# Kernel optimization log

Measured on AMD Instinct MI355X. Metric: run time of the kernel, lower is better.

Reference implementation:

```python
import jax, jax.numpy as jnp
import numpy as np

N_QUBITS = 10
DIM = 2 ** N_QUBITS          # quantum state dimension
N_LAYERS = 8                 # QAOA circuit depth
B, D_IN, D_HID = 8192, 1024, 2048


def _build_hamiltonians(key):
    """Faithful to _create_cost_hamiltonian / _create_mixer_hamiltonian."""
    k1, k2 = jax.random.split(key)
    # cost: random diagonal * 0.1 plus 100 nearest-neighbour real couplings * 0.05
    diag = (jax.random.normal(k1, (DIM,)) * 0.1).astype(jnp.complex64)
    Hc = jnp.zeros((DIM, DIM), jnp.complex64).at[jnp.arange(DIM), jnp.arange(DIM)].set(diag)
    i = jnp.arange(100)
    j = (i + 1) % DIM
    c = (jax.random.normal(k2, (100,)) * 0.05).astype(jnp.complex64)
    Hc = Hc.at[i, j].set(c).at[j, i].set(jnp.conj(c))
    # mixer: sum of Pauli-X on every qubit -> H[i, i^(1<<q)] += 1
    idx = jnp.arange(DIM)
    Hm = jnp.zeros((DIM, DIM), jnp.complex64)
    for q in range(N_QUBITS):
        Hm = Hm.at[idx, idx ^ (1 << q)].add(1.0)
    return Hc, Hm


def setup_inputs() -> dict:
    key = jax.random.key(0)
    ks = jax.random.split(key, 8)
    Hc, Hm = _build_hamiltonians(ks[0])
    s = lambda k, *sh: jax.random.normal(k, sh, jnp.float32)
    return {
        "x": s(ks[1], B, D_IN),
        "W1": s(ks[2], D_IN, D_HID) * 0.02, "b1": jnp.zeros((D_HID,), jnp.float32),
        "W2": s(ks[3], D_HID, D_HID // 2) * 0.02, "b2": jnp.zeros((D_HID // 2,), jnp.float32),
        "Wq": s(ks[4], N_QUBITS, D_HID // 2) * 0.02, "bq": jnp.zeros((D_HID // 2,), jnp.float32),
        "Wo": s(ks[5], D_HID // 2, D_IN) * 0.02, "bo": jnp.zeros((D_IN,), jnp.float32),
        "circuit_params": s(ks[6], 2 * N_LAYERS),
        "Hc": Hc, "Hm": Hm,
    }


def _qaoa_params(circuit_params, Hc, Hm):
    """QuantumApproximateOptimizer.optimize_parameters: layered unitary evolution
    then a projective measurement mapped to +/-1 parameters."""
    state = jnp.full((DIM,), 1.0 / np.sqrt(DIM), jnp.complex64)
    for l in range(N_LAYERS):  # small fixed layer count -> Python loop OK
        gamma = circuit_params[2 * l].astype(jnp.complex64)
        beta = circuit_params[2 * l + 1].astype(jnp.complex64)
        state = jax.scipy.linalg.expm(-1j * gamma * Hc) @ state
        state = jax.scipy.linalg.expm(-1j * beta * Hm) @ state
    probs = jnp.abs(state) ** 2
    m = jax.random.categorical(jax.random.key(42), jnp.log(probs + 1e-30))
    # format(m, '0{n}b') is MSB-first
    bits = (m >> jnp.arange(N_QUBITS - 1, -1, -1)) & 1
    return bits.astype(jnp.float32) * 2.0 - 1.0  # +/-1 per qubit


def reference(x, W1, b1, W2, b2, Wq, bq, Wo, bo, circuit_params, Hc, Hm):
    # classical encoder: Linear -> ReLU -> Linear
    feat = jax.nn.relu(x @ W1 + b1) @ W2 + b2          # [B, D_HID//2]
    # quantum branch (batch independent)
    qp = _qaoa_params(circuit_params, Hc, Hm)          # [N_QUBITS]
    # surface-code error correction: correction_lookup only maps syndromes
    # '0000'/'1111' to qubit indices 23/24, which fail the `qubit_idx < param_dim`
    # guard for param_dim = N_QUBITS -> provably a no-op; qp unchanged.
    qf = qp @ Wq + bq                                  # [D_HID//2]
    return (feat + qf) @ Wo + bo                       # [B, D_IN]
```

## Files before the change

### kernel.cpp

```cpp
#include <hip/hip_runtime.h>
#include <hip/hip_bf16.h>
#include <stdint.h>

#define DIM 1024
#define NQ 10
#define NLAYERS 8
#define KTAYLOR 24
#define B_ROWS 8192
#define D_IN 1024
#define D_HID 2048
#define D_HALF 1024

typedef __bf16 bf16x8 __attribute__((ext_vector_type(8)));
typedef float f32x4 __attribute__((ext_vector_type(4)));

__device__ __forceinline__ float ldany(const void* p, size_t i, bool f32) {
  if (f32) return ((const float*)p)[i];
  return (float)((const __bf16*)p)[i];
}

__device__ __forceinline__ uint16_t f2bf_bits(float f) {
  __bf16 v = (__bf16)f;
  return *(uint16_t*)&v;
}

__global__ void detect_kernel(const uint32_t* __restrict__ w1raw,
                              const uint32_t* __restrict__ hc,
                              int* __restrict__ flags) {
  if (threadIdx.x == 0) {
    int cnt = 0;
    for (int i = 0; i < 256; ++i) {
      uint16_t h = (uint16_t)(w1raw[i] & 0xFFFFu);
      if (((h >> 7) & 0xFF) >= 0x80) cnt++;
    }
    flags[0] = (cnt > 32) ? 1 : 0;

    uint32_t w1 = hc[1] & 0x7FFFFFFFu;
    uint32_t w2 = hc[2] & 0x7FFFFFFFu;
    uint32_t w1025 = hc[1025] & 0x7FFFFFFFu;
    int code;
    if (w2 != 0u) code = 1;
    else if (w1 != 0u && (w1 >> 16) == 0u) code = 3;
    else if (w1025 != 0u) code = 2;
    else if (w1 != 0u) code = 4;
    else code = 0;
    flags[1] = code;
  }
}

__global__ __launch_bounds__(256) void convert_bf16(
    const void* __restrict__ src, size_t soff, __bf16* __restrict__ dst,
    int n, const int* __restrict__ flags) {
  int i = (blockIdx.x * 256 + threadIdx.x) * 8;
  if (i >= n) return;
  if (flags[0]) {
    const float* s = (const float*)src + soff + i;
#pragma unroll
    for (int j = 0; j < 8; ++j) dst[i + j] = (__bf16)s[j];
  } else {
    *(uint4*)(dst + i) = *(const uint4*)((const uint16_t*)src + soff + i);
  }
}

__device__ __forceinline__ uint32_t rotl32(uint32_t v, int d) {
  return (v << d) | (v >> (32 - d));
}

__device__ inline void threefry2x32(uint32_t k0, uint32_t k1, uint32_t& x0, uint32_t& x1) {
  uint32_t ks2 = k0 ^ k1 ^ 0x1BD11BDAu;
  x0 += k0; x1 += k1;
#define RND(r) { x0 += x1; x1 = rotl32(x1, r); x1 ^= x0; }
  RND(13) RND(15) RND(26) RND(6)
  x0 += k1; x1 += ks2 + 1u;
  RND(17) RND(29) RND(16) RND(24)
  x0 += ks2; x1 += k0 + 2u;
  RND(13) RND(15) RND(26) RND(6)
  x0 += k0; x1 += k1 + 3u;
  RND(17) RND(29) RND(16) RND(24)
  x0 += k1; x1 += ks2 + 4u;
  RND(13) RND(15) RND(26) RND(6)
  x0 += ks2; x1 += k0 + 5u;
#undef RND
}

__device__ __forceinline__ float gumbel_from_bits(uint32_t b) {
  float f = __uint_as_float((b >> 9) | 0x3f800000u) - 1.0f;
  float u = fmaxf(f, 1.17549435e-38f);
  return -logf(-logf(u));
}

struct cplx { double r, i; };
__device__ __forceinline__ cplx load_hc(const void* H, int code, size_t idx) {
  switch (code) {
    case 2: return {(double)((const float*)H)[idx], 0.0};
    case 3: {
      const uint16_t* h = (const uint16_t*)H;
      return {(double)__uint_as_float((uint32_t)h[2 * idx] << 16),
              (double)__uint_as_float((uint32_t)h[2 * idx + 1] << 16)};
    }
    case 4: {
      const double* d = (const double*)H;
      return {d[2 * idx], d[2 * idx + 1]};
    }
    default: {
      float2 v = ((const float2*)H)[idx];
      return {(double)v.x, (double)v.y};
    }
  }
}

__global__ __launch_bounds__(1024) void qaoa_kernel(
    const void* __restrict__ Hc_raw, const void* __restrict__ cp,
    const void* __restrict__ b1, const void* __restrict__ b2,
    const void* __restrict__ bq, const void* __restrict__ bo,
    const void* __restrict__ Wq, const int* __restrict__ flags,
    float* __restrict__ b1f, float* __restrict__ bias2, float* __restrict__ bof,
    int* __restrict__ diag) {
  __shared__ double2 Sb[2][DIM];
  __shared__ float red_v[16];
  __shared__ int   red_i[16];
  __shared__ float red_p[16];
  __shared__ int bm_sh;

  const int t = threadIdx.x;
  const int lane = t & 63, wave = t >> 6;
  const bool f32 = (flags[0] != 0);
  const int code = flags[1];

  cplx dg = load_hc(Hc_raw, code, (size_t)t * DIM + t);

  cplx tdg0{0,0}, tdg1{0,0}, tcu0{0,0}, tcu1{0,0}, tcd0{0,0}, tcd1{0,0};
  if (wave == 0 && lane <= 50) {
    const size_t e0 = 2 * lane, e1 = 2 * lane + 1;
    tdg0 = load_hc(Hc_raw, code, e0 * DIM + e0);
    tdg1 = load_hc(Hc_raw, code, e1 * DIM + e1);
    if (e0 <= 100) tcu0 = load_hc(Hc_raw, code, e0 * DIM + e0 + 1);
    if (e1 <= 100) tcu1 = load_hc(Hc_raw, code, e1 * DIM + e1 + 1);
    if (e0 >= 1 && e0 <= 100) tcd0 = load_hc(Hc_raw, code, e0 * DIM + e0 - 1);
    if (e1 <= 100) tcd1 = load_hc(Hc_raw, code, e1 * DIM + e1 - 1);
  }

  double ar = 0.03125, ai = 0.0;

  for (int l = 0; l < NLAYERS; ++l) {
    const double gamma = (double)ldany(cp, 2 * l, f32);
    const double beta  = (double)ldany(cp, 2 * l + 1, f32);

    Sb[0][t] = make_double2(ar, ai);
    __syncthreads();
    if (t >= 102) {
      double sn, cs;
      sincos(gamma * dg.r, &sn, &cs);
      double sc_ = exp(gamma * dg.i);
      double nr = sc_ * (ar * cs + ai * sn);
      double ni = sc_ * (ai * cs - ar * sn);
      ar = nr; ai = ni;
    } else if (wave == 0) {
      double p0r = 0, p0i = 0, p1r = 0, p1i = 0;
      if (lane <= 50) {
        double2 v0 = Sb[0][2 * lane], v1 = Sb[0][2 * lane + 1];
        p0r = v0.x; p0i = v0.y; p1r = v1.x; p1i = v1.y;
      }
      double y0r = p0r, y0i = p0i, y1r = p1r, y1i = p1i;
#pragma unroll 4
      for (int k = 1; k <= KTAYLOR; ++k) {
        double dnr = __shfl_up(p1r, 1), dni = __shfl_up(p1i, 1);
        double upr = __shfl_down(p0r, 1), upi = __shfl_down(p0i, 1);
        double h0r = tdg0.r * p0r - tdg0.i * p0i + tcu0.r * p1r - tcu0.i * p1i
                   + tcd0.r * dnr - tcd0.i * dni;
        double h0i = tdg0.r * p0i + tdg0.i * p0r + tcu0.r * p1i + tcu0.i * p1r
                   + tcd0.r * dni + tcd0.i * dnr;
        double h1r = tdg1.r * p1r - tdg1.i * p1i + tcu1.r * upr - tcu1.i * upi
                   + tcd1.r * p0r - tcd1.i * p0i;
        double h1i = tdg1.r * p1i + tdg1.i * p1r + tcu1.r * upi + tcu1.i * upr
                   + tcd1.r * p0i + tcd1.i * p0r;
        double s = gamma / (double)k;
        p0r = s * h0i; p0i = -s * h0r;
        p1r = s * h1i; p1i = -s * h1r;
        y0r += p0r; y0i += p0i; y1r += p1r; y1i += p1i;
      }
      if (lane <= 50) {
        Sb[0][2 * lane]     = make_double2(y0r, y0i);
        Sb[0][2 * lane + 1] = make_double2(y1r, y1i);
      }
    }
    __syncthreads();
    if (t <= 101) { double2 v = Sb[0][t]; ar = v.x; ai = v.y; }

    const double cb = cos(beta), sb_ = sin(beta);
#pragma unroll
    for (int q = 0; q < 6; ++q) {
      double br_ = __shfl_xor(ar, 1 << q);
      double bi_ = __shfl_xor(ai, 1 << q);
      double nr = cb * ar + sb_ * bi_;
      double ni = cb * ai - sb_ * br_;
      ar = nr; ai = ni;
    }
    int s = 0;
#pragma unroll
    for (int q = 6; q < 10; ++q) {
      Sb[s][t] = make_double2(ar, ai);
      __syncthreads();
      double2 b = Sb[s][t ^ (1 << q)];
      double nr = cb * ar + sb_ * b.y;
      double ni = cb * ai - sb_ * b.x;
      ar = nr; ai = ni;
      s ^= 1;
    }
  }

  double prob = ar * ar + ai * ai;
  float pv = (float)prob;
  float score;
  {
    float logit = (float)log(prob + 1e-30);
    uint32_t x0 = 0u, x1 = (uint32_t)t;
    threefry2x32(0u, 42u, x0, x1);
    score = logit + gumbel_from_bits(x0 ^ x1);
  }
  int idx = t;
#pragma unroll
  for (int off = 32; off >= 1; off >>= 1) {
    float ov = __shfl_down(score, off);
    int oi = __shfl_down(idx, off);
    pv += __shfl_down(pv, off);
    if (ov > score) { score = ov; idx = oi; }
  }
  if (lane == 0) { red_v[wave] = score; red_i[wave] = idx; red_p[wave] = pv; }
  __syncthreads();
  if (t == 0) {
    float best = red_v[0]; int bm = red_i[0]; float total = red_p[0];
    for (int w = 1; w < 16; ++w) {
      total += red_p[w];
      if (red_v[w] > best) { best = red_v[w]; bm = red_i[w]; }
    }
    bm_sh = bm;
    diag[0] = (!(total > 0.99f && total < 1.01f)) ? 1 : 0;
    diag[1] = bm;
  }
  __syncthreads();
  const int m = bm_sh;

  float acc = ldany(b2, t, f32) + ldany(bq, t, f32);
#pragma unroll
  for (int k = 0; k < NQ; ++k) {
    float qp = ((m >> (9 - k)) & 1) ? 1.f : -1.f;
    acc += qp * ldany(Wq, k * D_HALF + t, f32);
  }
  bias2[t] = acc;
  bof[t] = ldany(bo, t, f32);
  b1f[t] = ldany(b1, t, f32);
  b1f[t + 1024] = ldany(b1, t + 1024, f32);
}

__global__ void sentinel_kernel(const int* __restrict__ flags,
                                const int* __restrict__ diag,
                                float* __restrict__ out) {
  if (threadIdx.x == 0 && (diag[0] || flags[1] == 0)) {
    out[0] = 1048576.0f + 4194304.0f * (float)diag[0]
           + 65536.0f * (float)flags[1] + 16.0f * (float)diag[1];
  }
}

__global__ __launch_bounds__(256) void transpose_any(
    const void* __restrict__ in, uint16_t* __restrict__ out, int R, int C,
    const int* __restrict__ flags) {
  __shared__ uint16_t tile[32][33];
  const bool f32 = (flags[0] != 0);
  int bc = blockIdx.x * 32, br = blockIdx.y * 32;
  int x = threadIdx.x, y = threadIdx.y;
#pragma unroll
  for (int i = 0; i < 4; ++i) {
    int r = y * 4 + i;
    size_t idx = (size_t)(br + r) * C + bc + x;
    tile[r][x] = f32 ? f2bf_bits(((const float*)in)[idx])
                     : ((const uint16_t*)in)[idx];
  }
  __syncthreads();
#pragma unroll
  for (int i = 0; i < 4; ++i) {
    int c = y * 4 + i;
    out[(size_t)(bc + c) * R + br + x] = tile[x][c];
  }
}

template <bool RELU, bool OUTF32>
__global__ __launch_bounds__(256) void gemm_bt(
    const __bf16* __restrict__ A, const __bf16* __restrict__ Bt,
    const float* __restrict__ bias, void* __restrict__ Cout,
    int N, int K) {
  __shared__ __bf16 Als[128 * 32];
  __shared__ __bf16 Bls[128 * 32];

  const int tid = threadIdx.x;
  const int wave = tid >> 6, lane = tid & 63;
  const int m0 = blockIdx.y * 128, n0 = blockIdx.x * 128;
  const int wm = (wave >> 1) * 64, wn = (wave & 1) * 64;
  const int lm = lane & 15, quad = lane >> 4;

  f32x4 acc[4][4] = {};

  for (int k0 = 0; k0 < K; k0 += 32) {
#pragma unroll
    for (int r = 0; r < 2; ++r) {
      int e = r * 2048 + wave * 512 + lane * 8;
      int row = e >> 5, col = e & 31;
      const __bf16* gp = A + (size_t)(m0 + row) * K + k0 + col;
      __builtin_amdgcn_global_load_lds(
          (const __attribute__((address_space(1))) void*)gp,
          (__attribute__((address_space(3))) void*)(Als + r * 2048 + wave * 512),
          16, 0, 0);
    }
#pragma unroll
    for (int r = 0; r < 2; ++r) {
      int e = r * 2048 + wave * 512 + lane * 8;
      int row = e >> 5, col = e & 31;
      const __bf16* gp = Bt + (size_t)(n0 + row) * K + k0 + col;
      __builtin_amdgcn_global_load_lds(
          (const __attribute__((address_space(1))) void*)gp,
          (__attribute__((address_space(3))) void*)(Bls + r * 2048 + wave * 512),
          16, 0, 0);
    }
    __syncthreads();

    bf16x8 af[4], bfr[4];
#pragma unroll
    for (int i = 0; i < 4; ++i)
      af[i] = *(const bf16x8*)(Als + (wm + i * 16 + lm) * 32 + quad * 8);
#pragma unroll
    for (int i = 0; i < 4; ++i)
      bfr[i] = *(const bf16x8*)(Bls + (wn + i * 16 + lm) * 32 + quad * 8);

#pragma unroll
    for (int mi = 0; mi < 4; ++mi)
#pragma unroll
      for (int ni = 0; ni < 4; ++ni)
        acc[mi][ni] = __builtin_amdgcn_mfma_f32_16x16x32_bf16(
            af[mi], bfr[ni], acc[mi][ni], 0, 0, 0);
    __syncthreads();
  }

#pragma unroll
  for (int mi = 0; mi < 4; ++mi) {
#pragma unroll
    for (int ni = 0; ni < 4; ++ni) {
      int col = n0 + wn + ni * 16 + lm;
      float bv = bias[col];
#pragma unroll
      for (int r = 0; r < 4; ++r) {
        int row = m0 + wm + mi * 16 + quad * 4 + r;
        float v = acc[mi][ni][r] + bv;
        if (RELU) v = fmaxf(v, 0.f);
        size_t oi = (size_t)row * N + col;
        if (OUTF32) ((float*)Cout)[oi] = v;
        else        ((__bf16*)Cout)[oi] = (__bf16)v;
      }
    }
  }
}

extern "C" void kernel_launch(void* const* d_in, const int* in_sizes, int n_in,
                              void* d_out, int out_size, void* d_ws, size_t ws_size,
                              hipStream_t stream) {
  const void* x  = d_in[0];
  const void* W1 = d_in[1];
  const void* b1 = d_in[2];
  const void* W2 = d_in[3];
  const void* b2 = d_in[4];
  const void* Wq = d_in[5];
  const void* bq = d_in[6];
  const void* Wo = d_in[7];
  const void* bo = d_in[8];
  const void* cp = d_in[9];
  const void* Hc = d_in[10];
  float* out = (float*)d_out;

  char* ws = (char*)d_ws;
  float* b1f   = (float*)ws;
  float* bias2 = (float*)(ws + 8192);
  float* bof   = (float*)(ws + 12288);
  int*   flags = (int*)(ws + 16384);
  int*   diag  = (int*)(ws + 16384 + 64);
  __bf16* W1T = (__bf16*)(ws + 20480);
  __bf16* W2T = W1T + (size_t)2048 * 1024;
  __bf16* WoT = W2T + (size_t)2048 * 1024;
  const size_t head = 20480 + 10485760;
  int R = B_ROWS;
  while (R > 128 && head + (size_t)R * 8192 > ws_size) R >>= 1;
  __bf16* xc   = (__bf16*)(ws + head);
  __bf16* Hbuf = xc + (size_t)R * 1024;
  __bf16* Fbuf = Hbuf + (size_t)R * 2048;

  detect_kernel<<<1, 64, 0, stream>>>((const uint32_t*)W1, (const uint32_t*)Hc, flags);

  qaoa_kernel<<<1, 1024, 0, stream>>>(Hc, cp, b1, b2, bq, bo, Wq, flags,
                                      b1f, bias2, bof, diag);

  transpose_any<<<dim3(2048 / 32, 1024 / 32), dim3(32, 8), 0, stream>>>(
      W1, (uint16_t*)W1T, 1024, 2048, flags);
  transpose_any<<<dim3(1024 / 32, 2048 / 32), dim3(32, 8), 0, stream>>>(
      W2, (uint16_t*)W2T, 2048, 1024, flags);
  transpose_any<<<dim3(1024 / 32, 1024 / 32), dim3(32, 8), 0, stream>>>(
      Wo, (uint16_t*)WoT, 1024, 1024, flags);

  for (int off = 0; off < B_ROWS; off += R) {
    int nconv = R * 1024;
    convert_bf16<<<(nconv / 8 + 255) / 256, 256, 0, stream>>>(
        x, (size_t)off * D_IN, xc, nconv, flags);
    gemm_bt<true, false><<<dim3(D_HID / 128, R / 128), 256, 0, stream>>>(
        xc, W1T, b1f, Hbuf, D_HID, D_IN);
    gemm_bt<false, false><<<dim3(D_HALF / 128, R / 128), 256, 0, stream>>>(
        Hbuf, W2T, bias2, Fbuf, D_HALF, D_HID);
    gemm_bt<false, true><<<dim3(D_IN / 128, R / 128), 256, 0, stream>>>(
        Fbuf, WoT, bof, out + (size_t)off * D_IN, D_IN, D_HALF);
  }

  sentinel_kernel<<<1, 64, 0, stream>>>(flags, diag, out);
}
```

Before: 326.3 us.

## Double-buffer LDS tiles in GEMM and remap blocks across XCDs

Uses two LDS buffers per operand so the next K tile is fetched with global_load_lds while MFMAs consume the current one, hiding load latency. Also remaps the flat workgroup index so consecutive tiles land on the same XCD, which should improve L2 reuse. This doubles LDS use per block and may lower occupancy, and the remap assumes the block count is divisible by 8.

```diff
diff --git a/kernel.cpp b/kernel.cpp
--- a/kernel.cpp
+++ b/kernel.cpp
@@ -284,52 +284,63 @@
   }
 }
 
+__device__ __forceinline__ void stage_tile(
+    const __bf16* __restrict__ G, int row0, int K, int k0,
+    __bf16* lds, int wave, int lane) {
+#pragma unroll
+  for (int r = 0; r < 2; ++r) {
+    int e = r * 2048 + wave * 512 + lane * 8;
+    int row = e >> 5, col = e & 31;
+    const __bf16* gp = G + (size_t)(row0 + row) * K + k0 + col;
+    __builtin_amdgcn_global_load_lds(
+        (const __attribute__((address_space(1))) void*)gp,
+        (__attribute__((address_space(3))) void*)(lds + r * 2048 + wave * 512),
+        16, 0, 0);
+  }
+}
+
 template <bool RELU, bool OUTF32>
 __global__ __launch_bounds__(256) void gemm_bt(
     const __bf16* __restrict__ A, const __bf16* __restrict__ Bt,
     const float* __restrict__ bias, void* __restrict__ Cout,
     int N, int K) {
-  __shared__ __bf16 Als[128 * 32];
-  __shared__ __bf16 Bls[128 * 32];
+  __shared__ __bf16 Als[2][128 * 32];
+  __shared__ __bf16 Bls[2][128 * 32];
 
   const int tid = threadIdx.x;
   const int wave = tid >> 6, lane = tid & 63;
-  const int m0 = blockIdx.y * 128, n0 = blockIdx.x * 128;
+
+  const int gx = gridDim.x;
+  const int nwg = gx * gridDim.y;
+  int flat = blockIdx.y * gx + blockIdx.x;
+  const int chunk = nwg >> 3;
+  flat = (flat & 7) * chunk + (flat >> 3);
+  const int m0 = (flat / gx) * 128, n0 = (flat % gx) * 128;
+
   const int wm = (wave >> 1) * 64, wn = (wave & 1) * 64;
   const int lm = lane & 15, quad = lane >> 4;
 
   f32x4 acc[4][4] = {};
 
-  for (int k0 = 0; k0 < K; k0 += 32) {
-#pragma unroll
-    for (int r = 0; r < 2; ++r) {
-      int e = r * 2048 + wave * 512 + lane * 8;
-      int row = e >> 5, col = e & 31;
-      const __bf16* gp = A + (size_t)(m0 + row) * K + k0 + col;
-      __builtin_amdgcn_global_load_lds(
-          (const __attribute__((address_space(1))) void*)gp,
-          (__attribute__((address_space(3))) void*)(Als + r * 2048 + wave * 512),
-          16, 0, 0);
-    }
-#pragma unroll
-    for (int r = 0; r < 2; ++r) {
-      int e = r * 2048 + wave * 512 + lane * 8;
-      int row = e >> 5, col = e & 31;
-      const __bf16* gp = Bt + (size_t)(n0 + row) * K + k0 + col;
-      __builtin_amdgcn_global_load_lds(
-          (const __attribute__((address_space(1))) void*)gp,
-          (__attribute__((address_space(3))) void*)(Bls + r * 2048 + wave * 512),
-          16, 0, 0);
-    }
-    __syncthreads();
+  const int nt = K >> 5;
+  stage_tile(A,  m0, K, 0, Als[0], wave, lane);
+  stage_tile(Bt, n0, K, 0, Bls[0], wave, lane);
+  __syncthreads();
+
+  for (int t = 0; t < nt; ++t) {
+    const int cur = t & 1;
+    if (t + 1 < nt) {
+      stage_tile(A,  m0, K, (t + 1) << 5, Als[cur ^ 1], wave, lane);
+      stage_tile(Bt, n0, K, (t + 1) << 5, Bls[cur ^ 1], wave, lane);
+    }
 
     bf16x8 af[4], bfr[4];
 #pragma unroll
     for (int i = 0; i < 4; ++i)
-      af[i] = *(const bf16x8*)(Als + (wm + i * 16 + lm) * 32 + quad * 8);
+      af[i] = *(const bf16x8*)(Als[cur] + (wm + i * 16 + lm) * 32 + quad * 8);
 #pragma unroll
     for (int i = 0; i < 4; ++i)
-      bfr[i] = *(const bf16x8*)(Bls + (wn + i * 16 + lm) * 32 + quad * 8);
+      bfr[i] = *(const bf16x8*)(Bls[cur] + (wn + i * 16 + lm) * 32 + quad * 8);
 
 #pragma unroll
     for (int mi = 0; mi < 4; ++mi)
@@ -337,6 +348,7 @@
       for (int ni = 0; ni < 4; ++ni)
         acc[mi][ni] = __builtin_amdgcn_mfma_f32_16x16x32_bf16(
             af[mi], bfr[ni], acc[mi][ni], 0, 0, 0);
+
     __syncthreads();
   }
 
```

Result: faster. 307.6 us (-5.7%).
